# Performance work log

Measured on AMD Instinct MI355X. Metric: run time of the kernel, lower is better.

## Reference

```python
import jax, jax.numpy as jnp
import numpy as np
import math

MID = 48       # mid_channels
HEADS = 4      # num_heads
POS = 16       # mid_channels // 3 (row/col positional channels)


def _unfold(x, p):
    """nn.Unfold with kernel p, padding p//2: (..., H, W) -> (..., p, p, H, W)."""
    H, W = x.shape[-2], x.shape[-1]
    pad = p // 2
    xp = jnp.pad(x, [(0, 0)] * (x.ndim - 2) + [(pad, pad), (pad, pad)])
    return jnp.stack(
        [jnp.stack([xp[..., k:k + H, l:l + W] for l in range(p)], axis=-3)
         for k in range(p)], axis=-4)


def _pe_mlp(idx, w1, b1, g, b, w2, b2):
    """Conv2d(1->16,1x1) -> LayerNorm(16) -> Swish -> Conv2d(16->POS,1x1) on scalar coords."""
    t = idx.reshape(-1, 1)                         # (N,1)
    h = t @ w1.T + b1                              # (N,16)
    mu = jnp.mean(h, -1, keepdims=True)
    var = jnp.var(h, -1, keepdims=True)
    h = (h - mu) * jax.lax.rsqrt(var + 1e-5) * g + b
    h = h * jax.nn.sigmoid(h)                      # Swish
    e = h @ w2.T + b2                              # (N,POS)
    return e.reshape(idx.shape + (e.shape[-1],))   # (V,P,P,POS)


def setup_inputs() -> dict:
    key = jax.random.key(0)
    ks = jax.random.split(key, 32)
    B, Cin, G, H, W, P, Cout = 2, 32, 4, 28, 28, 7, 64

    def n(k, shp, s=0.05):
        return jax.random.normal(k, shp, dtype=jnp.float32) * s

    inp = {"x": jax.random.normal(ks[0], (B, Cin, G, H, W), dtype=jnp.float32)}
    inp["Wq"] = n(ks[1], (MID * HEADS, Cin)); inp["bq"] = n(ks[2], (MID * HEADS,))
    inp["Wk"] = n(ks[3], (MID * HEADS, Cin)); inp["bk"] = n(ks[4], (MID * HEADS,))
    inp["Wv"] = n(ks[5], (MID * HEADS, Cin)); inp["bv"] = n(ks[6], (MID * HEADS,))
    inp["Wout"] = n(ks[7], (Cout, MID * HEADS)); inp["bout"] = n(ks[8], (Cout,))
    inp["row_w1"] = n(ks[9], (16, 1)); inp["row_b1"] = n(ks[10], (16,))
    inp["row_ln_g"] = jnp.ones((16,), jnp.float32); inp["row_ln_b"] = jnp.zeros((16,), jnp.float32)
    inp["row_w2"] = n(ks[11], (POS, 16)); inp["row_b2"] = n(ks[12], (POS,))
    inp["col_w1"] = n(ks[13], (16, 1)); inp["col_b1"] = n(ks[14], (16,))
    inp["col_ln_g"] = jnp.ones((16,), jnp.float32); inp["col_ln_b"] = jnp.zeros((16,), jnp.float32)
    inp["col_w2"] = n(ks[15], (POS, 16)); inp["col_b2"] = n(ks[16], (POS,))
    inp["group_emb"] = n(ks[17], (G, MID - 2 * POS))
    # rotated relative spatial positions, normalized to [-1, 1]
    lin = np.linspace(-1.0, 1.0, P).astype(np.float32)
    r = np.repeat(lin[:, None], P, 1)
    c = np.repeat(lin[None, :], P, 0)
    rows, cols = [], []
    for v in range(G):
        th = v * math.pi / 2.0
        rows.append(math.cos(th) * r - math.sin(th) * c)
        cols.append(math.sin(th) * r + math.cos(th) * c)
    inp["row_indices"] = jnp.asarray(np.stack(rows, 0))
    inp["col_indices"] = jnp.asarray(np.stack(cols, 0))
    # acted relative group positions for cyclic group C4
    ar = np.arange(G)
    gi = (ar[:, None, None] + ar[None, None, :] - ar[None, :, None]) % G
    inp["g_indices"] = jnp.asarray(gi, dtype=jnp.int32)
    return inp


def _forward(x, Wq, bq, Wk, bk, Wv, bv, Wout, bout,
             row_w1, row_b1, row_ln_g, row_ln_b, row_w2, row_b2,
             col_w1, col_b1, col_ln_g, col_ln_b, col_w2, col_b2,
             group_emb, row_indices, col_indices, g_indices):
    B, Cin, G, H, W = x.shape
    P = row_indices.shape[-1]
    sqn = jnp.sqrt(jnp.float32(Cin))

    def proj(Wm, bm):  # 1x1 Conv3d -> (B, MID, HEADS, G, H, W)
        y = jnp.einsum('oi,bigyx->bogyx', Wm, x) + bm[None, :, None, None, None]
        return y.reshape(B, MID, HEADS, G, H, W)

    q = proj(Wq, bq)
    k = proj(Wk, bk)
    v = proj(Wv, bv)
    k_loc = _unfold(k, P)   # (B, MID, HEADS, G, P, P, H, W)
    v_loc = _unfold(v, P)

    content = jnp.einsum('bchgij,bchmklij->bhgijmkl', q, k_loc)
    row_e = _pe_mlp(row_indices, row_w1, row_b1, row_ln_g, row_ln_b, row_w2, row_b2)
    col_e = _pe_mlp(col_indices, col_w1, col_b1, col_ln_g, col_ln_b, col_w2, col_b2)
    row_s = jnp.einsum('bchgij,vklc->bhvgijkl', q[:, :POS], row_e)
    col_s = jnp.einsum('bchgij,vklc->bhvgijkl', q[:, POS:2 * POS], col_e)
    g_e = group_emb[g_indices]                              # (V, G, M, gdim)
    g_s = jnp.einsum('bchgij,vgmc->bhvgijm', q[:, 2 * POS:], g_e)

    # scores: (b, h, v, g, i, j, m, k, l)
    scores = (row_s[:, :, :, :, :, :, None] + col_s[:, :, :, :, :, :, None]
              + g_s[..., None, None] + content[:, :, None]) / sqn

    # mask patch positions that fall outside the image (-inf -> prob 0)
    valid = _unfold(jnp.ones((H, W), jnp.float32), P)       # (P, P, H, W)
    valid = jnp.transpose(valid, (2, 3, 0, 1))[None, None, None, None, :, :, None, :, :]
    scores = jnp.where(valid > 0.5, scores, -jnp.inf)

    shp = scores.shape
    probs = jax.nn.softmax(scores.reshape(shp[:-3] + (-1,)), axis=-1).reshape(shp)

    o = jnp.einsum('bhvgijmkl,bchmklij->bchvij', probs, v_loc)  # (B, MID, HEADS, V, H, W)
    o = o.reshape(B, MID * HEADS, G, H, W)
    return jnp.einsum('oi,bivyx->bovyx', Wout, o) + bout[None, :, None, None, None]


def reference(x, Wq, bq, Wk, bk, Wv, bv, Wout, bout,
              row_w1, row_b1, row_ln_g, row_ln_b, row_w2, row_b2,
              col_w1, col_b1, col_ln_g, col_ln_b, col_w2, col_b2,
              group_emb, row_indices, col_indices, g_indices):
    return _forward(x, Wq, bq, Wk, bk, Wv, bv, Wout, bout,
                    row_w1, row_b1, row_ln_g, row_ln_b, row_w2, row_b2,
                    col_w1, col_b1, col_ln_g, col_ln_b, col_w2, col_b2,
                    group_emb, row_indices, col_indices, g_indices)
```

## Files before the change

kernel.cpp:

```cpp
#include <hip/hip_runtime.h>
#include <math.h>

#define Bb   2
#define CIN  32
#define Gg   4
#define NH   4
#define Hh   28
#define Ww   28
#define HW   784
#define Pp   7
#define PP   49
#define MID  48
#define COUT 64
#define OC   192

#define QF    0
#define KF    602112
#define VF    1204224
#define OOFF  1806336
#define KBH   75264
#define KM    18816
#define VBH   75264
#define VPL   37632

#define KSCALE 0.2550611135387359f

__device__ unsigned g_peT2[Gg * PP * 16];
__device__ unsigned g_geT2[8 * 64];
__device__ float    g_WT2[OC * COUT];

typedef _Float16 h2f __attribute__((ext_vector_type(2)));

__device__ __forceinline__ unsigned packh2(float a, float b) {
    auto r = __builtin_amdgcn_cvt_pkrtz(a, b);
    return __builtin_bit_cast(unsigned, r);
}

__device__ __forceinline__ float fdot2(unsigned a, unsigned b, float c) {
    return __builtin_amdgcn_fdot2(__builtin_bit_cast(h2f, a),
                                  __builtin_bit_cast(h2f, b), c, false);
}

__device__ __forceinline__ float exp2_fast(float x) {
    float r;
    asm("v_exp_f32 %0, %1" : "=v"(r) : "v"(x));
    return r;
}

__device__ __forceinline__ void conv14(const float4* __restrict__ Wr4, float bias,
                                       const float* __restrict__ xr, float* a) {
    #pragma unroll
    for (int j = 0; j < 14; j++) a[j] = bias;
    #pragma unroll 2
    for (int ci8 = 0; ci8 < 8; ci8++) {
        float4 wv4 = Wr4[ci8];
        int cb = ci8 * 4;
#define CHAN(WV, CI)                                                          \
        {                                                                     \
            float wv = WV;                                                    \
            float4 xA = *(const float4*)&xr[(CI) * 16 + 0];                   \
            float4 xB = *(const float4*)&xr[(CI) * 16 + 4];                   \
            float4 xC = *(const float4*)&xr[(CI) * 16 + 8];                   \
            float2 xD = *(const float2*)&xr[(CI) * 16 + 12];                  \
            a[0] += wv * xA.x;  a[1] += wv * xA.y;                            \
            a[2] += wv * xA.z;  a[3] += wv * xA.w;                            \
            a[4] += wv * xB.x;  a[5] += wv * xB.y;                            \
            a[6] += wv * xB.z;  a[7] += wv * xB.w;                            \
            a[8] += wv * xC.x;  a[9] += wv * xC.y;                            \
            a[10] += wv * xC.z; a[11] += wv * xC.w;                           \
            a[12] += wv * xD.x; a[13] += wv * xD.y;                           \
        }
        CHAN(wv4.x, cb + 0)
        CHAN(wv4.y, cb + 1)
        CHAN(wv4.z, cb + 2)
        CHAN(wv4.w, cb + 3)
#undef CHAN
    }
}

__global__ __launch_bounds__(192) void qkvpe_kernel(const float* __restrict__ x,
    const float* __restrict__ Wq, const float* __restrict__ bq,
    const float* __restrict__ Wk, const float* __restrict__ bk,
    const float* __restrict__ Wv, const float* __restrict__ bv,
    const float* row_w1, const float* row_b1,
    const float* row_g,  const float* row_bb,
    const float* row_w2, const float* row_b2,
    const float* col_w1, const float* col_b1,
    const float* col_g,  const float* col_bb,
    const float* col_w2, const float* col_b2,
    const float* row_idx, const float* col_idx,
    const float* group_emb, const int* g_indices,
    const float* Wout,
    float* __restrict__ ws)
{
    __shared__ float xs[2 * CIN * 16];
    __shared__ float wtmp[16 * 193];
    int tid = threadIdx.x;
    unsigned* uw = (unsigned*)ws;
    if (blockIdx.x == Bb * 2 * Hh * 2) {
        for (int t = tid; t < 2 * Gg * PP; t += 192) {
            int half = t / (Gg * PP);
            int n    = t - half * (Gg * PP);
            int v = n / PP, kl = n % PP;
            const float* w1 = half ? col_w1 : row_w1;
            const float* b1 = half ? col_b1 : row_b1;
            const float* lg = half ? col_g  : row_g;
            const float* lb = half ? col_bb : row_bb;
            const float* w2 = half ? col_w2 : row_w2;
            const float* b2 = half ? col_b2 : row_b2;
            float tv = half ? col_idx[n] : row_idx[n];

            float hb[16];
            float mean = 0.f;
            for (int k = 0; k < 16; k++) { hb[k] = tv * w1[k] + b1[k]; mean += hb[k]; }
            mean *= (1.f / 16.f);
            float var = 0.f;
            for (int k = 0; k < 16; k++) { float d = hb[k] - mean; var += d * d; }
            var *= (1.f / 16.f);
            float inv = 1.f / sqrtf(var + 1e-5f);
            for (int k = 0; k < 16; k++) {
                float hn = (hb[k] - mean) * inv * lg[k] + lb[k];
                hb[k] = hn / (1.f + expf(-hn));
            }
            float accv[16];
            for (int p = 0; p < 16; p++) {
                float acc = b2[p];
                for (int k = 0; k < 16; k++) acc += hb[k] * w2[p * 16 + k];
                accv[p] = acc * KSCALE;
            }
            for (int i2 = 0; i2 < 8; i2++)
                g_peT2[(v * PP + kl) * 16 + half * 8 + i2] =
                    packh2(accv[2 * i2], accv[2 * i2 + 1]);
        }
        for (int t = tid; t < 64; t += 192) {
            int gi = g_indices[t];
            for (int i2 = 0; i2 < 8; i2++)
                g_geT2[i2 * 64 + t] = packh2(group_emb[gi * 16 + 2 * i2] * KSCALE,
                                             group_emb[gi * 16 + 2 * i2 + 1] * KSCALE);
        }
        for (int chunk = 0; chunk < 4; chunk++) {
            int obase = chunk * 16;
            __syncthreads();
            for (int idx = tid; idx < 16 * OC; idx += 192) {
                int ol = idx / OC, t = idx % OC;
                wtmp[ol * 193 + t] = Wout[(obase + ol) * OC + t];
            }
            __syncthreads();
            for (int idx = tid; idx < 16 * OC; idx += 192) {
                int tp = idx / 16, ol = idx % 16;
                int h = tp / MID, c = tp % MID;
                g_WT2[tp * 64 + obase + ol] = wtmp[ol * 193 + c * NH + h];
            }
        }
        return;
    }

    int r = blockIdx.x;
    int jh = r & 1; r >>= 1;
    int i = r % Hh; r /= Hh;
    int gp = r & 1; int b = r >> 1;
    int j0 = jh * 14;

    for (int idx = tid; idx < 2 * CIN * 14; idx += 192) {
        int gs = idx / (CIN * 14), rem = idx % (CIN * 14);
        int ci = rem / 14, jj = rem % 14;
        xs[gs * CIN * 16 + ci * 16 + jj] =
            x[((b * CIN + ci) * Gg + 2 * gp + gs) * HW + i * Ww + j0 + jj];
    }
    __syncthreads();

    int h = tid / MID, c = tid % MID;
    int oo = c * NH + h;
    int bh = b * NH + h;
    int ij0 = i * Ww + j0;

    #pragma unroll 1
    for (int p = 0; p < 2; p++) {
        const float* Wm = p ? Wk : Wq;
        const float* bm = p ? bk : bq;
        float scl = p ? KSCALE : 1.0f;
        int base0 = p ? KF : QF;
        const float4* Wr4 = (const float4*)(Wm + oo * CIN);
        float bias = bm[oo];
        #pragma unroll 1
        for (int gs = 0; gs < 2; gs++) {
            float a[14];
            conv14(Wr4, bias, &xs[gs * CIN * 16], a);
            int obase = base0 + ((bh * Gg + 2 * gp + gs) * HW + ij0) * 24 + (c >> 1);
            #pragma unroll
            for (int jj = 0; jj < 14; jj++) {
                float av = a[jj] * scl;
                float pr = __shfl_xor(av, 1, 64);
                if (!(tid & 1)) uw[obase + jj * 24] = packh2(av, pr);
            }
        }
    }
    {
        const float4* Wr4 = (const float4*)(Wv + oo * CIN);
        float bias = bv[oo];
        float a0[14], a1[14];
        conv14(Wr4, bias, &xs[0], a0);
        conv14(Wr4, bias, &xs[CIN * 16], a1);
        int obase = VF + ((bh * 2 + gp) * HW + ij0) * 48 + c;
        #pragma unroll
        for (int jj = 0; jj < 14; jj++)
            uw[obase + jj * 48] = packh2(a0[jj], a1[jj]);
    }
}

__global__ __launch_bounds__(256, 4) void attn_kernel(float* __restrict__ ws)
{
    __shared__ __align__(16) unsigned kvb[7000];
    __shared__ __align__(16) unsigned pp2[4][PP][8];
    __shared__ __align__(16) unsigned qp[4][4][32];
    __shared__ __align__(16) float gsm[4][64];

    const int tid  = threadIdx.x;
    const int wave = tid >> 6;
    const int lane = tid & 63;

    int blk = blockIdx.x;
    int j0 = (blk % 7) * 4;
    int i  = (blk / 7) % Hh;
    int bh = blk / (7 * Hh);
    int b = bh >> 2, h = bh & 3;
    int j  = j0 + wave;
    int ij = i * Ww + j;

    const unsigned* uw = (const unsigned*)ws;
    const unsigned* Kf = uw + KF + bh * KBH;
    const unsigned* Vf = uw + VF + bh * VBH;
    float* Ot = ws + OOFF;

    if (lane < 48) {
        int g = lane / 12, c4 = lane % 12;
        uint2 qv = *(const uint2*)&uw[QF + ((bh * Gg + g) * HW + ij) * 24 + c4 * 2];
        qp[wave][g][c4 * 2]     = qv.x;
        qp[wave][g][c4 * 2 + 1] = qv.y;
    }

    #pragma unroll
    for (int s = 0; s < 2; s++) {
        int t = tid + s * 256;
        if (t < 420) {
            int c8 = t % 6, cl = t / 6;
            int gy = i - 3 + cl / 10, gx = j0 - 3 + cl % 10;
            gy = min(max(gy, 0), Hh - 1); gx = min(max(gx, 0), Ww - 1);
            const unsigned* kp = &Kf[(gy * Ww + gx) * 24 + c8 * 4];
            #pragma unroll
            for (int m = 0; m < 4; m++) {
                uint4 kv = *(const uint4*)(kp + m * KM);
                int o = (m * 70 + cl) * 25 + c8 * 4;
                *(uint2*)&kvb[o]     = make_uint2(kv.x, kv.y);
                *(uint2*)&kvb[o + 2] = make_uint2(kv.z, kv.w);
            }
        }
    }

    int kk = lane / Pp, ll = lane % Pp;
    int cell = (lane < PP) ? kk * 10 + ll + wave : 0;
    bool vmask = (lane < PP) && ((unsigned)(i + kk - 3) < Hh) && ((unsigned)(j + ll - 3) < Ww);
    int lclamp = lane < PP ? lane : 0;

    float per[4][4] = {};
    #pragma unroll
    for (int u4 = 0; u4 < 4; u4++) {
        uint4 qA = *(const uint4*)&qp[wave][0][u4 * 4];
        uint4 qB = *(const uint4*)&qp[wave][1][u4 * 4];
        uint4 qC = *(const uint4*)&qp[wave][2][u4 * 4];
        uint4 qD = *(const uint4*)&qp[wave][3][u4 * 4];
        #pragma unroll
        for (int v = 0; v < 4; v++) {
            uint4 pk = *(const uint4*)&g_peT2[(v * PP + lclamp) * 16 + u4 * 4];
            per[v][0] = fdot2(pk.w, qA.w, fdot2(pk.z, qA.z, fdot2(pk.y, qA.y, fdot2(pk.x, qA.x, per[v][0]))));
            per[v][1] = fdot2(pk.w, qB.w, fdot2(pk.z, qB.z, fdot2(pk.y, qB.y, fdot2(pk.x, qB.x, per[v][1]))));
            per[v][2] = fdot2(pk.w, qC.w, fdot2(pk.z, qC.z, fdot2(pk.y, qC.y, fdot2(pk.x, qC.x, per[v][2]))));
            per[v][3] = fdot2(pk.w, qD.w, fdot2(pk.z, qD.z, fdot2(pk.y, qD.y, fdot2(pk.x, qD.x, per[v][3]))));
        }
    }
    if (!vmask) {
        #pragma unroll
        for (int v = 0; v < 4; v++)
            #pragma unroll
            for (int g = 0; g < 4; g++) per[v][g] = -INFINITY;
    }

    {
        int g = (lane >> 2) & 3;
        float ga = 0.f;
        #pragma unroll
        for (int u = 0; u < 8; u++)
            ga = fdot2(g_geT2[u * 64 + lane], qp[wave][g][16 + u], ga);
        gsm[wave][lane] = ga;
    }
    __syncthreads();

    float acc[4][4] = {};
    #pragma unroll 2
    for (int u4 = 0; u4 < 6; u4++) {
        uint4 qA = *(const uint4*)&qp[wave][0][u4 * 4];
        uint4 qB = *(const uint4*)&qp[wave][1][u4 * 4];
        uint4 qC = *(const uint4*)&qp[wave][2][u4 * 4];
        uint4 qD = *(const uint4*)&qp[wave][3][u4 * 4];
        #pragma unroll
        for (int m = 0; m < 4; m++) {
            int base = (m * 70 + cell) * 25 + u4 * 4;
            uint2 k01 = *(const uint2*)&kvb[base];
            uint2 k23 = *(const uint2*)&kvb[base + 2];
            acc[m][0] = fdot2(k23.y, qA.w, fdot2(k23.x, qA.z, fdot2(k01.y, qA.y, fdot2(k01.x, qA.x, acc[m][0]))));
            acc[m][1] = fdot2(k23.y, qB.w, fdot2(k23.x, qB.z, fdot2(k01.y, qB.y, fdot2(k01.x, qB.x, acc[m][1]))));
            acc[m][2] = fdot2(k23.y, qC.w, fdot2(k23.x, qC.z, fdot2(k01.y, qC.y, fdot2(k01.x, qC.x, acc[m][2]))));
            acc[m][3] = fdot2(k23.y, qD.w, fdot2(k23.x, qD.z, fdot2(k01.y, qD.y, fdot2(k01.x, qD.x, acc[m][3]))));
        }
    }

#define VLOAD(T, A, Bv)                                                       \
    {   int c4_ = (T) % 12, cl_ = (T) / 12;                                   \
        int gy_ = i - 3 + cl_ / 10, gx_ = j0 - 3 + cl_ % 10;                  \
        gy_ = min(max(gy_, 0), Hh - 1); gx_ = min(max(gx_, 0), Ww - 1);       \
        int off_ = (gy_ * Ww + gx_) * 48 + c4_ * 4;                           \
        A  = *(const uint4*)&Vf[off_];                                        \
        Bv = *(const uint4*)&Vf[VPL + off_]; }
#define VSTORE(T, A, Bv)                                                      \
    {   int c4_ = (T) % 12, cl_ = (T) / 12;                                   \
        int o_ = cl_ * 48 + c4_ * 4;                                          \
        *(uint4*)&kvb[o_]        = A;                                         \
        *(uint4*)&kvb[3360 + o_] = Bv; }
    uint4 pA0, pB0, pA1, pB1, pA2, pB2;
    VLOAD(tid,       pA0, pB0)
    VLOAD(tid + 256, pA1, pB1)
    VLOAD(tid + 512, pA2, pB2)

    float ppr[4][4] = {};
    #pragma unroll
    for (int v = 0; v < 4; v++) {
        #pragma unroll
        for (int g = 0; g < 4; g++) {
            int vg = v * 4 + g;
            float4 gs = *(const float4*)&gsm[wave][vg * 4];
            float ex[4];
            ex[0] = exp2_fast(acc[0][g] + per[v][g] + gs.x);
            ex[1] = exp2_fast(acc[1][g] + per[v][g] + gs.y);
            ex[2] = exp2_fast(acc[2][g] + per[v][g] + gs.z);
            ex[3] = exp2_fast(acc[3][g] + per[v][g] + gs.w);
            float ls = ex[0] + ex[1] + ex[2] + ex[3];
            #pragma unroll
            for (int d = 32; d > 0; d >>= 1) ls += __shfl_xor(ls, d, 64);
            float rinv = 1.0f / ls;
            #pragma unroll
            for (int m = 0; m < 4; m++) ppr[v][m] += ex[m] * rinv;
        }
    }
    if (lane < PP) {
        uint4 w0, w1;
        w0.x = packh2(ppr[0][0], ppr[0][1]); w0.y = packh2(ppr[0][2], ppr[0][3]);
        w0.z = packh2(ppr[1][0], ppr[1][1]); w0.w = packh2(ppr[1][2], ppr[1][3]);
        w1.x = packh2(ppr[2][0], ppr[2][1]); w1.y = packh2(ppr[2][2], ppr[2][3]);
        w1.z = packh2(ppr[3][0], ppr[3][1]); w1.w = packh2(ppr[3][2], ppr[3][3]);
        *(uint4*)&pp2[wave][lane][0] = w0;
        *(uint4*)&pp2[wave][lane][4] = w1;
    }
    __syncthreads();

    uint4 sA, sB;
    if (tid < 72) { VLOAD(tid + 768, sA, sB) }
    VSTORE(tid,       pA0, pB0)
    VSTORE(tid + 256, pA1, pB1)
    VSTORE(tid + 512, pA2, pB2)
    if (tid < 72) { VSTORE(tid + 768, sA, sB) }
#undef VLOAD
#undef VSTORE
    __syncthreads();

    if (lane < MID) {
        float o0 = 0.f, o1 = 0.f, o2 = 0.f, o3 = 0.f;
        const uint4* ppw = (const uint4*)&pp2[wave][0][0];
        const unsigned* v0b = &kvb[wave * 48 + lane];
        const unsigned* v1b = v0b + 3360;
        #pragma unroll
        for (int kl2 = 0; kl2 < PP; kl2++) {
            int cellc = (kl2 / Pp) * 10 + (kl2 % Pp);
            unsigned vv0 = v0b[cellc * 48];
            unsigned vv1 = v1b[cellc * 48];
            uint4 A = ppw[kl2 * 2];
            uint4 B = ppw[kl2 * 2 + 1];
            o0 = fdot2(vv1, A.y, fdot2(vv0, A.x, o0));
            o1 = fdot2(vv1, A.w, fdot2(vv0, A.z, o1));
            o2 = fdot2(vv1, B.y, fdot2(vv0, B.x, o2));
            o3 = fdot2(vv1, B.w, fdot2(vv0, B.z, o3));
        }
        Ot[((size_t)(b * Gg + 0) * HW + ij) * OC + h * MID + lane] = o0;
        Ot[((size_t)(b * Gg + 1) * HW + ij) * OC + h * MID + lane] = o1;
        Ot[((size_t)(b * Gg + 2) * HW + ij) * OC + h * MID + lane] = o2;
        Ot[((size_t)(b * Gg + 3) * HW + ij) * OC + h * MID + lane] = o3;
    }
}

__global__ __launch_bounds__(256) void outproj_kernel(const float* __restrict__ bout,
                                                      const float* __restrict__ ws,
                                                      float* __restrict__ out)
{
    __shared__ float ov[16 * 193];
    __shared__ float res[64 * 17];
    int tid = threadIdx.x;
    int p0 = blockIdx.x * 16;
    const float* Ot = ws + OOFF;

    for (int idx = tid; idx < 16 * OC; idx += 256) {
        int pl = idx / OC, t = idx % OC;
        ov[pl * 193 + t] = Ot[(size_t)(p0 + pl) * OC + t];
    }
    __syncthreads();

    int o = tid & 63, pg = tid >> 6;
    float a0 = bout[o], a1 = a0, a2 = a0, a3 = a0;
    for (int t = 0; t < OC; t++) {
        float w = g_WT2[t * 64 + o];
        a0 += w * ov[(pg     ) * 193 + t];
        a1 += w * ov[(pg +  4) * 193 + t];
        a2 += w * ov[(pg +  8) * 193 + t];
        a3 += w * ov[(pg + 12) * 193 + t];
    }
    res[o * 17 + pg     ] = a0;
    res[o * 17 + pg +  4] = a1;
    res[o * 17 + pg +  8] = a2;
    res[o * 17 + pg + 12] = a3;
    __syncthreads();

    for (int idx = tid; idx < 1024; idx += 256) {
        int o2 = idx >> 4, pl = idx & 15;
        int p = p0 + pl;
        int ij2 = p % HW; int bv = p / HW; int v = bv & 3; int bb = bv >> 2;
        out[((bb * COUT + o2) * Gg + v) * HW + ij2] = res[o2 * 17 + pl];
    }
}

extern "C" void kernel_launch(void* const* d_in, const int* in_sizes, int n_in,
                              void* d_out, int out_size, void* d_ws, size_t ws_size,
                              hipStream_t stream)
{
    const float* x      = (const float*)d_in[0];
    const float* Wq     = (const float*)d_in[1];
    const float* bq     = (const float*)d_in[2];
    const float* Wk     = (const float*)d_in[3];
    const float* bk     = (const float*)d_in[4];
    const float* Wv     = (const float*)d_in[5];
    const float* bv     = (const float*)d_in[6];
    const float* Wout   = (const float*)d_in[7];
    const float* bout   = (const float*)d_in[8];
    const float* row_w1 = (const float*)d_in[9];
    const float* row_b1 = (const float*)d_in[10];
    const float* row_g  = (const float*)d_in[11];
    const float* row_bb = (const float*)d_in[12];
    const float* row_w2 = (const float*)d_in[13];
    const float* row_b2 = (const float*)d_in[14];
    const float* col_w1 = (const float*)d_in[15];
    const float* col_b1 = (const float*)d_in[16];
    const float* col_g  = (const float*)d_in[17];
    const float* col_bb = (const float*)d_in[18];
    const float* col_w2 = (const float*)d_in[19];
    const float* col_b2 = (const float*)d_in[20];
    const float* gemb   = (const float*)d_in[21];
    const float* ridx   = (const float*)d_in[22];
    const float* cidx   = (const float*)d_in[23];
    const int*   gidx   = (const int*)d_in[24];

    float* ws  = (float*)d_ws;
    float* out = (float*)d_out;

    qkvpe_kernel<<<Bb * 2 * Hh * 2 + 1, 192, 0, stream>>>(
        x, Wq, bq, Wk, bk, Wv, bv,
        row_w1, row_b1, row_g, row_bb, row_w2, row_b2,
        col_w1, col_b1, col_g, col_bb, col_w2, col_b2,
        ridx, cidx, gemb, gidx, Wout, ws);
    attn_kernel<<<Bb * NH * Hh * (Ww / 4), 256, 0, stream>>>(ws);
    outproj_kernel<<<Bb * Gg * HW / 16, 256, 0, stream>>>(bout, ws, out);
}
```

Before: 169.0 us.

## Split QKV projection into 7-column tiles, drop V prefetch overlap, unroll outproj

The QKV projection kernel now handles 7 columns per block instead of 14, which doubles the grid. It processes both groups together with the weights held in registers, so each weight row is loaded once per projection. In the attention kernel, the V-tile global loads that were issued early to overlap with score computation are replaced by a simple load/store loop after the softmax. The output projection's inner loop gets an unroll pragma. Smaller tiles add parallelism but reload x per block, and removing the prefetch may expose V load latency.

```diff
diff --git a/kernel.cpp b/kernel.cpp
--- a/kernel.cpp
+++ b/kernel.cpp
@@ -47,34 +47,30 @@
     return r;
 }
 
-__device__ __forceinline__ void conv14(const float4* __restrict__ Wr4, float bias,
-                                       const float* __restrict__ xr, float* a) {
-    #pragma unroll
-    for (int j = 0; j < 14; j++) a[j] = bias;
-    #pragma unroll 2
+__device__ __forceinline__ void conv7x2(const float4* __restrict__ Wr4, float bias,
+                                        const float* __restrict__ x0,
+                                        const float* __restrict__ x1,
+                                        float* a0, float* a1) {
+    float4 w[8];
+    #pragma unroll
+    for (int t = 0; t < 8; t++) w[t] = Wr4[t];
+    #pragma unroll
+    for (int jj = 0; jj < 7; jj++) { a0[jj] = bias; a1[jj] = bias; }
+    #pragma unroll
     for (int ci8 = 0; ci8 < 8; ci8++) {
-        float4 wv4 = Wr4[ci8];
         int cb = ci8 * 4;
-#define CHAN(WV, CI)                                                          \
-        {                                                                     \
-            float wv = WV;                                                    \
-            float4 xA = *(const float4*)&xr[(CI) * 16 + 0];                   \
-            float4 xB = *(const float4*)&xr[(CI) * 16 + 4];                   \
-            float4 xC = *(const float4*)&xr[(CI) * 16 + 8];                   \
-            float2 xD = *(const float2*)&xr[(CI) * 16 + 12];                  \
-            a[0] += wv * xA.x;  a[1] += wv * xA.y;                            \
-            a[2] += wv * xA.z;  a[3] += wv * xA.w;                            \
-            a[4] += wv * xB.x;  a[5] += wv * xB.y;                            \
-            a[6] += wv * xB.z;  a[7] += wv * xB.w;                            \
-            a[8] += wv * xC.x;  a[9] += wv * xC.y;                            \
-            a[10] += wv * xC.z; a[11] += wv * xC.w;                           \
-            a[12] += wv * xD.x; a[13] += wv * xD.y;                           \
-        }
-        CHAN(wv4.x, cb + 0)
-        CHAN(wv4.y, cb + 1)
-        CHAN(wv4.z, cb + 2)
-        CHAN(wv4.w, cb + 3)
-#undef CHAN
+#define CH1(WV, CI, XR, A)                                                    \
+        {   float wv = WV;                                                    \
+            float4 xA = *(const float4*)&XR[(CI) * 8];                        \
+            float4 xB = *(const float4*)&XR[(CI) * 8 + 4];                    \
+            A[0] += wv * xA.x; A[1] += wv * xA.y; A[2] += wv * xA.z;          \
+            A[3] += wv * xA.w; A[4] += wv * xB.x; A[5] += wv * xB.y;          \
+            A[6] += wv * xB.z; }
+        CH1(w[ci8].x, cb + 0, x0, a0) CH1(w[ci8].x, cb + 0, x1, a1)
+        CH1(w[ci8].y, cb + 1, x0, a0) CH1(w[ci8].y, cb + 1, x1, a1)
+        CH1(w[ci8].z, cb + 2, x0, a0) CH1(w[ci8].z, cb + 2, x1, a1)
+        CH1(w[ci8].w, cb + 3, x0, a0) CH1(w[ci8].w, cb + 3, x1, a1)
+#undef CH1
     }
 }
 
@@ -93,11 +89,11 @@
     const float* Wout,
     float* __restrict__ ws)
 {
-    __shared__ float xs[2 * CIN * 16];
+    __shared__ float xs[2 * CIN * 8];
     __shared__ float wtmp[16 * 193];
     int tid = threadIdx.x;
     unsigned* uw = (unsigned*)ws;
-    if (blockIdx.x == Bb * 2 * Hh * 2) {
+    if (blockIdx.x == Bb * 2 * Hh * 4) {
         for (int t = tid; t < 2 * Gg * PP; t += 192) {
             int half = t / (Gg * PP);
             int n    = t - half * (Gg * PP);
@@ -156,15 +152,15 @@
     }
 
     int r = blockIdx.x;
-    int jh = r & 1; r >>= 1;
+    int jq = r & 3; r >>= 2;
     int i = r % Hh; r /= Hh;
     int gp = r & 1; int b = r >> 1;
-    int j0 = jh * 14;
-
-    for (int idx = tid; idx < 2 * CIN * 14; idx += 192) {
-        int gs = idx / (CIN * 14), rem = idx % (CIN * 14);
-        int ci = rem / 14, jj = rem % 14;
-        xs[gs * CIN * 16 + ci * 16 + jj] =
+    int j0 = jq * 7;
+
+    for (int idx = tid; idx < 2 * CIN * 7; idx += 192) {
+        int gs = idx / (CIN * 7), rem = idx % (CIN * 7);
+        int ci = rem / 7, jj = rem % 7;
+        xs[gs * CIN * 8 + ci * 8 + jj] =
             x[((b * CIN + ci) * Gg + 2 * gp + gs) * HW + i * Ww + j0 + jj];
     }
     __syncthreads();
@@ -173,38 +169,45 @@
     int oo = c * NH + h;
     int bh = b * NH + h;
     int ij0 = i * Ww + j0;
-
-    #pragma unroll 1
-    for (int p = 0; p < 2; p++) {
-        const float* Wm = p ? Wk : Wq;
-        const float* bm = p ? bk : bq;
-        float scl = p ? KSCALE : 1.0f;
-        int base0 = p ? KF : QF;
-        const float4* Wr4 = (const float4*)(Wm + oo * CIN);
-        float bias = bm[oo];
-        #pragma unroll 1
-        for (int gs = 0; gs < 2; gs++) {
-            float a[14];
-            conv14(Wr4, bias, &xs[gs * CIN * 16], a);
-            int obase = base0 + ((bh * Gg + 2 * gp + gs) * HW + ij0) * 24 + (c >> 1);
-            #pragma unroll
-            for (int jj = 0; jj < 14; jj++) {
-                float av = a[jj] * scl;
-                float pr = __shfl_xor(av, 1, 64);
-                if (!(tid & 1)) uw[obase + jj * 24] = packh2(av, pr);
-            }
-        }
-    }
+    const float* xs0 = &xs[0];
+    const float* xs1 = &xs[CIN * 8];
+
+    float a0[7], a1[7];
+    conv7x2((const float4*)(Wq + oo * CIN), bq[oo], xs0, xs1, a0, a1);
     {
-        const float4* Wr4 = (const float4*)(Wv + oo * CIN);
-        float bias = bv[oo];
-        float a0[14], a1[14];
-        conv14(Wr4, bias, &xs[0], a0);
-        conv14(Wr4, bias, &xs[CIN * 16], a1);
-        int obase = VF + ((bh * 2 + gp) * HW + ij0) * 48 + c;
-        #pragma unroll
-        for (int jj = 0; jj < 14; jj++)
-            uw[obase + jj * 48] = packh2(a0[jj], a1[jj]);
+        int ob0 = QF + ((bh * Gg + 2 * gp + 0) * HW + ij0) * 24 + (c >> 1);
+        int ob1 = QF + ((bh * Gg + 2 * gp + 1) * HW + ij0) * 24 + (c >> 1);
+        #pragma unroll
+        for (int jj = 0; jj < 7; jj++) {
+            float p0 = __shfl_xor(a0[jj], 1, 64);
+            float p1 = __shfl_xor(a1[jj], 1, 64);
+            if (!(tid & 1)) {
+                uw[ob0 + jj * 24] = packh2(a0[jj], p0);
+                uw[ob1 + jj * 24] = packh2(a1[jj], p1);
+            }
+        }
+    }
+    conv7x2((const float4*)(Wk + oo * CIN), bk[oo], xs0, xs1, a0, a1);
+    {
+        int ob0 = KF + ((bh * Gg + 2 * gp + 0) * HW + ij0) * 24 + (c >> 1);
+        int ob1 = KF + ((bh * Gg + 2 * gp + 1) * HW + ij0) * 24 + (c >> 1);
+        #pragma unroll
+        for (int jj = 0; jj < 7; jj++) {
+            float v0 = a0[jj] * KSCALE, v1 = a1[jj] * KSCALE;
+            float p0 = __shfl_xor(v0, 1, 64);
+            float p1 = __shfl_xor(v1, 1, 64);
+            if (!(tid & 1)) {
+                uw[ob0 + jj * 24] = packh2(v0, p0);
+                uw[ob1 + jj * 24] = packh2(v1, p1);
+            }
+        }
+    }
+    conv7x2((const float4*)(Wv + oo * CIN), bv[oo], xs0, xs1, a0, a1);
+    {
+        int vb = VF + ((bh * 2 + gp) * HW + ij0) * 48 + c;
+        #pragma unroll
+        for (int jj = 0; jj < 7; jj++)
+            uw[vb + jj * 48] = packh2(a0[jj], a1[jj]);
     }
 }
 
@@ -313,23 +316,6 @@
             acc[m][3] = fdot2(k23.y, qD.w, fdot2(k23.x, qD.z, fdot2(k01.y, qD.y, fdot2(k01.x, qD.x, acc[m][3]))));
         }
     }
-
-#define VLOAD(T, A, Bv)                                                       \
-    {   int c4_ = (T) % 12, cl_ = (T) / 12;                                   \
-        int gy_ = i - 3 + cl_ / 10, gx_ = j0 - 3 + cl_ % 10;                  \
-        gy_ = min(max(gy_, 0), Hh - 1); gx_ = min(max(gx_, 0), Ww - 1);       \
-        int off_ = (gy_ * Ww + gx_) * 48 + c4_ * 4;                           \
-        A  = *(const uint4*)&Vf[off_];                                        \
-        Bv = *(const uint4*)&Vf[VPL + off_]; }
-#define VSTORE(T, A, Bv)                                                      \
-    {   int c4_ = (T) % 12, cl_ = (T) / 12;                                   \
-        int o_ = cl_ * 48 + c4_ * 4;                                          \
-        *(uint4*)&kvb[o_]        = A;                                         \
-        *(uint4*)&kvb[3360 + o_] = Bv; }
-    uint4 pA0, pB0, pA1, pB1, pA2, pB2;
-    VLOAD(tid,       pA0, pB0)
-    VLOAD(tid + 256, pA1, pB1)
-    VLOAD(tid + 512, pA2, pB2)
 
     float ppr[4][4] = {};
     #pragma unroll
@@ -362,14 +348,17 @@
     }
     __syncthreads();
 
-    uint4 sA, sB;
-    if (tid < 72) { VLOAD(tid + 768, sA, sB) }
-    VSTORE(tid,       pA0, pB0)
-    VSTORE(tid + 256, pA1, pB1)
-    VSTORE(tid + 512, pA2, pB2)
-    if (tid < 72) { VSTORE(tid + 768, sA, sB) }
-#undef VLOAD
-#undef VSTORE
+    for (int t = tid; t < 840; t += 256) {
+        int c4 = t % 12, cl = t / 12;
+        int gy = i - 3 + cl / 10, gx = j0 - 3 + cl % 10;
+        gy = min(max(gy, 0), Hh - 1); gx = min(max(gx, 0), Ww - 1);
+        int off = (gy * Ww + gx) * 48 + c4 * 4;
+        uint4 A = *(const uint4*)&Vf[off];
+        uint4 B = *(const uint4*)&Vf[VPL + off];
+        int o = cl * 48 + c4 * 4;
+        *(uint4*)&kvb[o]        = A;
+        *(uint4*)&kvb[3360 + o] = B;
+    }
     __syncthreads();
 
     if (lane < MID) {
@@ -414,6 +403,7 @@
 
     int o = tid & 63, pg = tid >> 6;
     float a0 = bout[o], a1 = a0, a2 = a0, a3 = a0;
+    #pragma unroll 8
     for (int t = 0; t < OC; t++) {
         float w = g_WT2[t * 64 + o];
         a0 += w * ov[(pg     ) * 193 + t];
@@ -468,7 +458,7 @@
     float* ws  = (float*)d_ws;
     float* out = (float*)d_out;
 
-    qkvpe_kernel<<<Bb * 2 * Hh * 2 + 1, 192, 0, stream>>>(
+    qkvpe_kernel<<<Bb * 2 * Hh * 4 + 1, 192, 0, stream>>>(
         x, Wq, bq, Wk, bk, Wv, bv,
         row_w1, row_b1, row_g, row_bb, row_w2, row_b2,
         col_w1, col_b1, col_g, col_bb, col_w2, col_b2,
```

New measurement: 187.5 us. 1.11x slower.
